# Kernel tuning notes

Measured on AMD Instinct MI355X. Metric: run time of the kernel, lower is better.

The kernel has to match this reference:

```python
import jax, jax.numpy as jnp
import numpy as np

TEMPERATURE = 8.0  # init_kwargs temperature
NEG_INF = -1e16


def setup_inputs() -> dict:
    key = jax.random.key(0)
    ks = jax.random.split(key, 8)
    B, S, D = 4, 1024, 64
    q = jax.random.normal(ks[0], (B, S, D), dtype=jnp.float32)
    k = jax.random.normal(ks[1], (B, S, D), dtype=jnp.float32)
    v = jax.random.normal(ks[2], (B, S, D), dtype=jnp.float32)
    # MLP params (Linear(2D,50) -> ReLU -> Linear(50,25) -> ReLU -> Linear(25,1))
    W1 = jax.random.normal(ks[3], (2 * D, 50), dtype=jnp.float32) * (1.0 / np.sqrt(2 * D))
    b1 = jnp.zeros((50,), dtype=jnp.float32)
    W2 = jax.random.normal(ks[4], (50, 25), dtype=jnp.float32) * (1.0 / np.sqrt(50))
    b2 = jnp.zeros((25,), dtype=jnp.float32)
    W3 = jax.random.normal(ks[5], (25, 1), dtype=jnp.float32) * (1.0 / np.sqrt(25))
    b3 = jnp.zeros((1,), dtype=jnp.float32)
    # causal mask: True where attention is disallowed (j > i)
    mask = jnp.triu(jnp.ones((S, S), dtype=bool), k=1)
    mask = jnp.broadcast_to(mask, (B, S, S))
    return {"q": q, "k": k, "v": v, "W1": W1, "b1": b1, "W2": W2,
            "b2": b2, "W3": W3, "b3": b3, "mask": mask}


def reference(q, k, v, W1, b1, W2, b2, W3, b3, mask):
    D = q.shape[-1]
    # cat([q_i, k_j]) @ W1 == q_i @ W1[:D] + k_j @ W1[D:]; avoids the
    # explicit [B,S,S,2D] concat the torch code materializes.
    Wq, Wk = W1[:D], W1[D:]
    hq = jnp.einsum('bsd,df->bsf', q, Wq)           # [B,S,50]
    hk = jnp.einsum('btd,df->btf', k, Wk)           # [B,S,50]
    h1 = jax.nn.relu(hq[:, :, None, :] + hk[:, None, :, :] + b1)  # [B,S,S,50]
    h2 = jax.nn.relu(jnp.einsum('bstf,fg->bstg', h1, W2) + b2)    # [B,S,S,25]
    scores = (jnp.einsum('bstg,go->bsto', h2, W3) + b3)[..., 0]    # [B,S,S]
    scores = scores / TEMPERATURE
    scores = jnp.where(mask, NEG_INF, scores)
    attn = jax.nn.softmax(scores, axis=2)           # softmax over key dim
    out = jnp.einsum('bst,btd->bsd', attn, v)       # [B,S,D]
    return (out, attn)
```

## Files before the change

kernel.cpp:

```cpp
#include <hip/hip_runtime.h>
#include <hip/hip_bf16.h>
#include <math.h>

#define BB 4
#define SQL 1024
#define DD 64
#define NFP 64
#define TEMP_INV 0.125f

typedef __attribute__((ext_vector_type(8))) short bf16x8;
typedef __attribute__((ext_vector_type(4))) float f32x4;

__device__ __forceinline__ short f2bf(float f) {
  __hip_bfloat16 h = __float2bfloat16(f);
  return *reinterpret_cast<short*>(&h);
}

__global__ __launch_bounds__(64) void proj_kernel(
    const float* __restrict__ q, const float* __restrict__ k,
    const float* __restrict__ W1, const float* __restrict__ b1,
    float* __restrict__ hq, float* __restrict__ hk)
{
  int row = blockIdx.x;
  int isK = blockIdx.y;
  int f = threadIdx.x;
  __shared__ float r[DD];
  const float* src = isK ? k : q;
  r[f] = src[row * DD + f];
  __syncthreads();
  float acc = 0.f;
  if (f < 50) {
    acc = isK ? 0.f : b1[f];
    const float* w = W1 + isK * DD * 50 + f;
#pragma unroll
    for (int d = 0; d < DD; ++d) acc = fmaf(r[d], w[d * 50], acc);
  }
  float* dst = isK ? hk : hq;
  dst[row * NFP + f] = acc;
}

__global__ __launch_bounds__(256) void attn_kernel(
    const float* __restrict__ hq, const float* __restrict__ hk,
    const float* __restrict__ v,
    const float* __restrict__ W2, const float* __restrict__ b2,
    const float* __restrict__ W3, const float* __restrict__ b3,
    float* __restrict__ out, float* __restrict__ attn)
{
  const int bid  = blockIdx.x;
  const int b    = blockIdx.y;
  const int tid  = threadIdx.x;
  const int lane = tid & 63;
  const int wave = tid >> 6;
  const int lo   = lane & 15;
  const int grp  = lane >> 4;

  __shared__ float sc[8][SQL];
  __shared__ float shq[8][NFP];

  const int sA = 4 * bid;
  const int sB = 1020 - 4 * bid;

  if (tid < 128) {
    int r = tid >> 4, q4 = (tid & 15) * 4;
    int s = (r < 4) ? (sA + r) : (sB + r - 4);
    *(float4*)(&shq[r][q4]) =
        *(const float4*)(hq + ((size_t)(b * SQL + s)) * NFP + q4);
  }

  bf16x8 w2f[2][2];
#pragma unroll
  for (int gt = 0; gt < 2; ++gt) {
    int g = lo + 16 * gt;
#pragma unroll
    for (int c = 0; c < 2; ++c) {
      bf16x8 fr;
#pragma unroll
      for (int j = 0; j < 8; ++j) {
        int f = c * 32 + grp * 8 + j;
        float val = (f < 50 && g < 25) ? W2[f * 25 + g] : 0.f;
        fr[j] = f2bf(val);
      }
      w2f[gt][c] = fr;
    }
  }
  float w3a[4], w3b[4], b2a[4], b2b[4];
#pragma unroll
  for (int rr = 0; rr < 4; ++rr) {
    int g0 = grp * 4 + rr;
    int g1 = 16 + grp * 4 + rr;
    w3a[rr] = W3[g0];
    b2a[rr] = b2[g0];
    w3b[rr] = (g1 < 25) ? W3[g1] : 0.f;
    b2b[rr] = (g1 < 25) ? b2[g1] : 0.f;
  }
  const float b3v = b3[0];

  __syncthreads();

  const int smax = sB + 3;
  const int ntiles = (smax >> 5) + 1;
  const float* hkb = hk + (size_t)b * SQL * NFP;

  for (int tt = wave; tt < ntiles; tt += 4) {
    const int tbase = tt << 5;
    float hkv[2][2][8];
#pragma unroll
    for (int th = 0; th < 2; ++th) {
      const float* p = hkb + (size_t)(tbase + th * 16 + lo) * NFP + grp * 8;
#pragma unroll
      for (int c = 0; c < 2; ++c) {
        *(float4*)&hkv[th][c][0] = *(const float4*)(p + c * 32);
        *(float4*)&hkv[th][c][4] = *(const float4*)(p + c * 32 + 4);
      }
    }
#pragma unroll 1
    for (int r = 0; r < 8; ++r) {
      const int s = (r < 4) ? (sA + r) : (sB + r - 4);
      if (s < tbase) continue;
      float hqv[2][8];
#pragma unroll
      for (int c = 0; c < 2; ++c) {
        *(float4*)&hqv[c][0] = *(const float4*)(&shq[r][c * 32 + grp * 8]);
        *(float4*)&hqv[c][4] = *(const float4*)(&shq[r][c * 32 + grp * 8 + 4]);
      }
      f32x4 acc[2][2] = {{{0.f,0.f,0.f,0.f},{0.f,0.f,0.f,0.f}},
                         {{0.f,0.f,0.f,0.f},{0.f,0.f,0.f,0.f}}};
#pragma unroll
      for (int th = 0; th < 2; ++th) {
#pragma unroll
        for (int c = 0; c < 2; ++c) {
          bf16x8 bfrag;
#pragma unroll
          for (int j = 0; j < 8; ++j)
            bfrag[j] = f2bf(fmaxf(hqv[c][j] + hkv[th][c][j], 0.f));
          acc[th][0] = __builtin_amdgcn_mfma_f32_16x16x32_bf16(w2f[0][c], bfrag, acc[th][0], 0, 0, 0);
          acc[th][1] = __builtin_amdgcn_mfma_f32_16x16x32_bf16(w2f[1][c], bfrag, acc[th][1], 0, 0, 0);
        }
      }
#pragma unroll
      for (int th = 0; th < 2; ++th) {
        float part = 0.f;
#pragma unroll
        for (int rr = 0; rr < 4; ++rr) {
          part += fmaxf(acc[th][0][rr] + b2a[rr], 0.f) * w3a[rr];
          part += fmaxf(acc[th][1][rr] + b2b[rr], 0.f) * w3b[rr];
        }
        part += __shfl_xor(part, 16);
        part += __shfl_xor(part, 32);
        float score = (part + b3v) * TEMP_INV;
        if (lane < 16) sc[r][tbase + th * 16 + lane] = score;
      }
    }
  }

  __syncthreads();

  for (int r = wave; r < 8; r += 4) {
    const int s = (r < 4) ? (sA + r) : (sB + r - 4);
    float vv[16];
#pragma unroll
    for (int c = 0; c < 16; ++c) {
      int t = c * 64 + lane;
      vv[c] = (t <= s) ? sc[r][t] : -INFINITY;
    }
    float m = vv[0];
#pragma unroll
    for (int c = 1; c < 16; ++c) m = fmaxf(m, vv[c]);
#pragma unroll
    for (int off = 32; off; off >>= 1) m = fmaxf(m, __shfl_xor(m, off));
    float sum = 0.f;
#pragma unroll
    for (int c = 0; c < 16; ++c) {
      float e = (c * 64 + lane <= s) ? __expf(vv[c] - m) : 0.f;
      vv[c] = e;
      sum += e;
    }
#pragma unroll
    for (int off = 32; off; off >>= 1) sum += __shfl_xor(sum, off);
    const float inv = 1.f / sum;
    float* arow = attn + ((size_t)(b * SQL + s)) * SQL;
#pragma unroll
    for (int c = 0; c < 16; ++c) {
      float a = vv[c] * inv;
      arow[c * 64 + lane] = a;
      sc[r][c * 64 + lane] = a;
    }
    const float* vb = v + (size_t)(b * SQL) * DD + lane;
    float acc = 0.f;
    int t = 0;
    for (; t + 3 <= s; t += 4) {
      float a0 = sc[r][t], a1 = sc[r][t + 1], a2 = sc[r][t + 2], a3 = sc[r][t + 3];
      acc = fmaf(a0, vb[(size_t)t * DD], acc);
      acc = fmaf(a1, vb[(size_t)(t + 1) * DD], acc);
      acc = fmaf(a2, vb[(size_t)(t + 2) * DD], acc);
      acc = fmaf(a3, vb[(size_t)(t + 3) * DD], acc);
    }
    for (; t <= s; ++t) acc = fmaf(sc[r][t], vb[(size_t)t * DD], acc);
    out[((size_t)(b * SQL + s)) * DD + lane] = acc;
  }
}

extern "C" void kernel_launch(void* const* d_in, const int* in_sizes, int n_in,
                              void* d_out, int out_size, void* d_ws, size_t ws_size,
                              hipStream_t stream) {
  const float* q  = (const float*)d_in[0];
  const float* k  = (const float*)d_in[1];
  const float* v  = (const float*)d_in[2];
  const float* W1 = (const float*)d_in[3];
  const float* b1 = (const float*)d_in[4];
  const float* W2 = (const float*)d_in[5];
  const float* b2 = (const float*)d_in[6];
  const float* W3 = (const float*)d_in[7];
  const float* b3 = (const float*)d_in[8];

  float* out  = (float*)d_out;
  float* attn = out + BB * SQL * DD;

  float* hq = (float*)d_ws;
  float* hk = hq + BB * SQL * NFP;

  proj_kernel<<<dim3(BB * SQL, 2), 64, 0, stream>>>(q, k, W1, b1, hq, hk);
  attn_kernel<<<dim3(128, BB), 256, 0, stream>>>(hq, hk, v, W2, b2, W3, b3, out, attn);
}
```

Before: 188.6 us.

## Double waves per attention block and pack four rows per projection block

The attention kernel now runs 512 threads (8 waves) per block instead of 256. The key tiles are split across 8 waves, and each wave handles exactly one query row in the softmax and PV phase, so the per-wave serial work is halved. The projection kernel packs four rows into each 256-thread block to cut the launch block count, and the PV accumulation uses four independent accumulators to break the FMA dependency chain. The larger blocks raise register pressure under launch_bounds(512,4), and the block-level LDS footprint is unchanged.

```diff
diff --git a/kernel.cpp b/kernel.cpp
--- a/kernel.cpp
+++ b/kernel.cpp
@@ -16,30 +16,32 @@
   return *reinterpret_cast<short*>(&h);
 }
 
-__global__ __launch_bounds__(64) void proj_kernel(
+__global__ __launch_bounds__(256) void proj_kernel(
     const float* __restrict__ q, const float* __restrict__ k,
     const float* __restrict__ W1, const float* __restrict__ b1,
     float* __restrict__ hq, float* __restrict__ hk)
 {
-  int row = blockIdx.x;
-  int isK = blockIdx.y;
-  int f = threadIdx.x;
-  __shared__ float r[DD];
+  const int lane = threadIdx.x & 63;
+  const int wave = threadIdx.x >> 6;
+  const int unit = blockIdx.x * 4 + wave;
+  const int isK  = unit >> 12;
+  const int row  = unit & 4095;
+  __shared__ float r[4][DD];
   const float* src = isK ? k : q;
-  r[f] = src[row * DD + f];
+  r[wave][lane] = src[row * DD + lane];
   __syncthreads();
   float acc = 0.f;
-  if (f < 50) {
-    acc = isK ? 0.f : b1[f];
-    const float* w = W1 + isK * DD * 50 + f;
-#pragma unroll
-    for (int d = 0; d < DD; ++d) acc = fmaf(r[d], w[d * 50], acc);
+  if (lane < 50) {
+    acc = isK ? 0.f : b1[lane];
+    const float* w = W1 + isK * DD * 50 + lane;
+#pragma unroll
+    for (int d = 0; d < DD; ++d) acc = fmaf(r[wave][d], w[d * 50], acc);
   }
   float* dst = isK ? hk : hq;
-  dst[row * NFP + f] = acc;
-}
-
-__global__ __launch_bounds__(256) void attn_kernel(
+  dst[row * NFP + lane] = acc;
+}
+
+__global__ __launch_bounds__(512, 4) void attn_kernel(
     const float* __restrict__ hq, const float* __restrict__ hk,
     const float* __restrict__ v,
     const float* __restrict__ W2, const float* __restrict__ b2,
@@ -101,7 +103,7 @@
   const int ntiles = (smax >> 5) + 1;
   const float* hkb = hk + (size_t)b * SQL * NFP;
 
-  for (int tt = wave; tt < ntiles; tt += 4) {
+  for (int tt = wave; tt < ntiles; tt += 8) {
     const int tbase = tt << 5;
     float hkv[2][2][8];
 #pragma unroll
@@ -155,7 +157,8 @@
 
   __syncthreads();
 
-  for (int r = wave; r < 8; r += 4) {
+  {
+    const int r = wave;
     const int s = (r < 4) ? (sA + r) : (sB + r - 4);
     float vv[16];
 #pragma unroll
@@ -186,17 +189,16 @@
       sc[r][c * 64 + lane] = a;
     }
     const float* vb = v + (size_t)(b * SQL) * DD + lane;
-    float acc = 0.f;
+    float a0 = 0.f, a1 = 0.f, a2 = 0.f, a3 = 0.f;
     int t = 0;
     for (; t + 3 <= s; t += 4) {
-      float a0 = sc[r][t], a1 = sc[r][t + 1], a2 = sc[r][t + 2], a3 = sc[r][t + 3];
-      acc = fmaf(a0, vb[(size_t)t * DD], acc);
-      acc = fmaf(a1, vb[(size_t)(t + 1) * DD], acc);
-      acc = fmaf(a2, vb[(size_t)(t + 2) * DD], acc);
-      acc = fmaf(a3, vb[(size_t)(t + 3) * DD], acc);
-    }
-    for (; t <= s; ++t) acc = fmaf(sc[r][t], vb[(size_t)t * DD], acc);
-    out[((size_t)(b * SQL + s)) * DD + lane] = acc;
+      a0 = fmaf(sc[r][t],     vb[(size_t)(t)     * DD], a0);
+      a1 = fmaf(sc[r][t + 1], vb[(size_t)(t + 1) * DD], a1);
+      a2 = fmaf(sc[r][t + 2], vb[(size_t)(t + 2) * DD], a2);
+      a3 = fmaf(sc[r][t + 3], vb[(size_t)(t + 3) * DD], a3);
+    }
+    for (; t <= s; ++t) a0 = fmaf(sc[r][t], vb[(size_t)t * DD], a0);
+    out[((size_t)(b * SQL + s)) * DD + lane] = (a0 + a1) + (a2 + a3);
   }
 }
 
@@ -219,6 +221,6 @@
   float* hq = (float*)d_ws;
   float* hk = hq + BB * SQL * NFP;
 
-  proj_kernel<<<dim3(BB * SQL, 2), 64, 0, stream>>>(q, k, W1, b1, hq, hk);
-  attn_kernel<<<dim3(128, BB), 256, 0, stream>>>(hq, hk, v, W2, b2, W3, b3, out, attn);
-}
+  proj_kernel<<<dim3(2048), 256, 0, stream>>>(q, k, W1, b1, hq, hk);
+  attn_kernel<<<dim3(128, BB), 512, 0, stream>>>(hq, hk, v, W2, b2, W3, b3, out, attn);
+}
```

Result: faster. 180.5 us (-4.3%).
